# Optimization experiments

Hardware: AMD Instinct MI355X
Metric: run time of the kernel (lower is better)

The kernel has to match this reference:

```python
import jax, jax.numpy as jnp
import numpy as np

N, V, F, H, B, HID = 256, 32, 128, 8, 8, 64
R_MAX = 5.0
DH = F // H


def fc_edges(n):
    a = np.arange(n)
    s, r = np.meshgrid(a, a, indexing="ij")
    m = s != r
    return jnp.asarray(s[m]), jnp.asarray(r[m])

SENDERS, RECEIVERS = fc_edges(N)
E = N * (N - 1)


def sph_harmonics(u):
    # u: [..., 3] unit vectors -> [..., 15] = l=1(3)+l=2(5)+l=3(7), e3nn 'component' normalization
    x, y, z = u[..., 0], u[..., 1], u[..., 2]
    s3 = 3.0 ** 0.5; s5 = 5.0 ** 0.5; s7 = 7.0 ** 0.5
    s15 = 15.0 ** 0.5; s105 = 105.0 ** 0.5
    s35_8 = (35.0 / 8.0) ** 0.5; s21_8 = (21.0 / 8.0) ** 0.5
    l1 = [s3 * y, s3 * z, s3 * x]
    l2 = [s15 * x * y, s15 * y * z, 0.5 * s5 * (3 * z * z - 1),
          s15 * x * z, 0.5 * s15 * (x * x - y * y)]
    l3 = [s35_8 * y * (3 * x * x - y * y), s105 * x * y * z,
          s21_8 * y * (5 * z * z - 1), 0.5 * s7 * z * (5 * z * z - 3),
          s21_8 * x * (5 * z * z - 1), 0.5 * s105 * z * (x * x - y * y),
          s35_8 * x * (x * x - 3 * y * y)]
    return jnp.stack(l1 + l2 + l3, axis=-1)


def radial_embed(lengths):
    # Bessel basis (e3nn.bessel) times soft envelope (e3nn.soft_envelope)
    x = jnp.maximum(lengths, 1e-6)[..., None]
    k = jnp.arange(1, B + 1, dtype=lengths.dtype)
    bes = (2.0 / R_MAX) ** 0.5 * jnp.sin(k * jnp.pi * x / R_MAX) / x
    def sus(t):
        return jnp.where(t > 0, jnp.exp(-1.0 / jnp.where(t > 0, t, 1.0)), 0.0)
    env = 1.2 * sus(2.0 * (1.0 - lengths / R_MAX)) / sus(jnp.asarray(2.0))
    return bes * env[..., None]


def setup_inputs():
    key = jax.random.key(0)
    ks = jax.random.split(key, 16)
    def w(k, shape):
        return jax.random.normal(k, shape, jnp.float32) / (shape[0] ** 0.5)
    D_edge = 2 * F + V * B
    return {
        "positions": jax.random.normal(ks[0], (N, V, 3), jnp.float32),
        "features": jax.random.normal(ks[1], (N, F), jnp.float32),
        "We1": w(ks[2], (D_edge, HID)), "be1": jnp.zeros((HID,), jnp.float32),
        "We2": w(ks[3], (HID, HID)), "be2": jnp.zeros((HID,), jnp.float32),
        "W_q": w(ks[4], (F, F)), "W_k": w(ks[5], (HID, F)),
        "W_v": w(ks[6], (F, F)), "W_vec": w(ks[7], (HID, V)),
        "W_mix": w(ks[8], (V, V)),
        "M1": w(ks[9], (F, HID)), "bm1": jnp.zeros((HID,), jnp.float32),
        "M2": w(ks[10], (HID, HID)), "bm2": jnp.zeros((HID,), jnp.float32),
        "M3": w(ks[11], (HID, F)), "bm3": jnp.zeros((F,), jnp.float32),
    }


def reference(positions, features, We1, be1, We2, be2, W_q, W_k, W_v, W_vec,
              W_mix, M1, bm1, M2, bm2, M3, bm3):
    act = jax.nn.selu
    s, r = SENDERS, RECEIVERS
    vectors = positions[s] - positions[r]                        # [E, V, 3]
    lengths = jnp.sqrt(jnp.sum(vectors * vectors, -1) + 1e-18)   # [E, V] safe_norm
    unit = vectors / lengths[..., None]
    sph = sph_harmonics(unit)                                    # [E, V, 15]
    radial = radial_embed(lengths).reshape(E, V * B)             # [E, V*B]
    edge_weight_cutoff = jnp.ones((E,), positions.dtype)

    # edge MLP on invariants (radial embedding + src/dst scalar features)
    edge_in = jnp.concatenate([features[s], features[r], radial], -1)
    h = act(edge_in @ We1 + be1)
    h = act(h @ We2 + be2)                                       # [E, HID]

    # multi-head attention over incoming edges per node (segment softmax)
    q = (features @ W_q).reshape(N, H, DH)
    k = (h @ W_k).reshape(E, H, DH)
    logit = jnp.einsum("ehd,ehd->eh", k, q[r]) / (DH ** 0.5)
    lmax = jax.ops.segment_max(logit, r, num_segments=N)
    ex = edge_weight_cutoff[:, None] * jnp.exp(logit - lmax[r])
    denom = jax.ops.segment_sum(ex, r, num_segments=N)
    alpha = ex / (denom[r] + 1e-12)                              # [E, H]

    # invariant (0e) values
    v = (features[s] @ W_v).reshape(E, H, DH)
    inv_agg = jax.ops.segment_sum(alpha[..., None] * v, r, num_segments=N).reshape(N, F)

    # equivariant (1o) values: scalar-gated l=1 spherical harmonics (sqrt(3)*unit)
    coeff = h @ W_vec                                            # [E, V]
    alpha_v = jnp.repeat(alpha, V // H, axis=1)                  # [E, V]
    vec_msg = ((alpha_v * coeff) * (3.0 ** 0.5))[..., None] * unit  # [E, V, 3]
    vec_agg = jax.ops.segment_sum(vec_msg, r, num_segments=N)    # [N, V, 3]
    vec_out = jnp.einsum("nvc,vw->nwc", vec_agg, W_mix)

    # final invariant MLP + residuals
    hi = act(inv_agg @ M1 + bm1)
    hi = act(hi @ M2 + bm2)
    inv_out = hi @ M3 + bm3
    return (vec_out + positions, inv_out + features)
```

## Files before the change

kernel.cpp:

```cpp
#include <hip/hip_runtime.h>
#include <hip/hip_bf16.h>

#define NN 256
#define VC 32
#define FD 128

typedef unsigned int uint32;
typedef unsigned short u16;
typedef __attribute__((ext_vector_type(8))) short bf16x8;
typedef __attribute__((ext_vector_type(4))) float f32x4;

__device__ __forceinline__ float selu_f(float x) {
    const float lam = 1.0507009873554805f;
    const float la  = 1.7580993408473766f;
    return x > 0.f ? lam * x : la * (__expf(x) - 1.f);
}

__device__ __forceinline__ u16 f32_to_bf16_rne(float f) {
    uint32 u = __float_as_uint(f);
    uint32 r = (u + 0x7fffu + ((u >> 16) & 1u)) >> 16;
    return (u16)r;
}

__device__ __forceinline__ float bf16_to_f32(u16 h) {
    return __uint_as_float(((uint32)h) << 16);
}

struct Params {
    const float *pos, *feat, *We1, *be1, *We2, *be2, *Wq, *Wk, *Wv, *Wvec,
                *Wmix, *M1, *bm1, *M2, *bm2, *M3, *bm3;
    float *A, *Bf;
    u16 *kqb, *w1b, *we2b, *wvb, *fvtH, *fvtL, *ptH, *ptL;
    float *lgg2;
    u16 *cfg2;
    float *inv, *vec4;
    float *out0, *out1;
};

__global__ __launch_bounds__(256) void k1_pre(Params P)
{
    __shared__ float fl[FD];
    __shared__ float ql[FD];
    const int vb = blockIdx.x;
    const int t = threadIdx.x;
    if (vb < 256) {
        const int n = vb;
        {
            const int gid = n*256 + t;
            if (gid < 16384) {
                const int c = gid >> 8, k = gid & 255;
                P.w1b[gid] = f32_to_bf16_rne(P.We1[(256 + k)*64 + c]);
            } else if (gid < 20480) {
                const int o = gid - 16384;
                const int c = o >> 6, k = o & 63;
                P.we2b[o] = f32_to_bf16_rne(P.We2[k*64 + c]);
            } else if (gid < 22528) {
                const int o = gid - 20480;
                const int v = o >> 6, k = o & 63;
                P.wvb[o] = f32_to_bf16_rne(P.Wvec[k*32 + v]);
            }
        }
        if (t < FD) fl[t] = P.feat[n*FD + t];
        __syncthreads();
        if (t < 64) {
            float a = 0.f;
            for (int i = 0; i < FD; ++i) a = fmaf(fl[i], P.We1[i*64 + t], a);
            P.A[n*64 + t] = a;
        } else if (t < 128) {
            const int j = t - 64;
            float a = P.be1[j];
            for (int i = 0; i < FD; ++i) a = fmaf(fl[i], P.We1[(FD+i)*64 + j], a);
            P.Bf[n*64 + j] = a;
        } else {
            const int j = t - 128;
            float a = 0.f;
            for (int i = 0; i < FD; ++i) a = fmaf(fl[i], P.Wq[i*FD + j], a);
            ql[j] = a * 0.25f;
        }
        if (t < 8)  P.lgg2[n*2048 + t*256 + n] = -1e30f;
        if (t < 32) P.cfg2[(size_t)n*8192 + t*256 + n] = 0;
        __syncthreads();
        for (int o = t; o < 512; o += 256) {
            const int h = o >> 6, j = o & 63;
            float a = 0.f;
            #pragma unroll
            for (int d = 0; d < 16; ++d)
                a = fmaf(P.Wk[j*FD + h*16 + d], ql[h*16 + d], a);
            P.kqb[n*512 + o] = f32_to_bf16_rne(a);
        }
    } else {
        const int n = vb - 256;
        if (t < FD) fl[t] = P.feat[n*FD + t];
        __syncthreads();
        if (t < FD) {
            float a = 0.f;
            for (int i = 0; i < FD; ++i) a = fmaf(fl[i], P.Wv[i*FD + t], a);
            const u16 hi = f32_to_bf16_rne(a);
            const u16 lo = f32_to_bf16_rne(a - bf16_to_f32(hi));
            P.fvtH[t*256 + n] = hi;
            P.fvtL[t*256 + n] = lo;
            const int v = t >> 2, c = t & 3;
            const float val = (c < 3) ? P.pos[(n*VC + v)*3 + c] : 1.0f;
            const u16 phi = f32_to_bf16_rne(val);
            const u16 plo = f32_to_bf16_rne(val - bf16_to_f32(phi));
            P.ptH[(v*4+c)*256 + n] = phi;
            P.ptL[(v*4+c)*256 + n] = plo;
        }
    }
}

__global__ __launch_bounds__(256) void k2_edge(Params P)
{
    __shared__ u16 rad[8192];
    __shared__ u16 h1b[2048];
    __shared__ u16 h2b[2048];
    __shared__ float invl[1056];

    const int t = threadIdx.x;
    const int wave = t >> 6, l = t & 63;
    const int li = l & 15, q = l >> 4;
    const int mh = wave >> 1, eh = wave & 1;
    const int r = blockIdx.x >> 1, tpart = blockIdx.x & 1;
    const int e = eh*16 + li;
    const int swz16 = (e & 7) << 3;

    bf16x8 w1A[2][8];
    #pragma unroll
    for (int mt = 0; mt < 2; ++mt) {
        const int c = mh*32 + mt*16 + li;
        #pragma unroll
        for (int kb = 0; kb < 8; ++kb)
            w1A[mt][kb] = *(const bf16x8*)(P.w1b + c*256 + kb*32 + q*8);
    }
    bf16x8 we2A[2][2];
    #pragma unroll
    for (int mt = 0; mt < 2; ++mt) {
        const int c2 = mh*32 + mt*16 + li;
        #pragma unroll
        for (int kb = 0; kb < 2; ++kb)
            we2A[mt][kb] = *(const bf16x8*)(P.we2b + c2*64 + kb*32 + q*8);
    }
    bf16x8 wvA[2];
    {
        const int v = mh*16 + li;
        #pragma unroll
        for (int kb = 0; kb < 2; ++kb)
            wvA[kb] = *(const bf16x8*)(P.wvb + v*64 + kb*32 + q*8);
    }
    bf16x8 kqA[2];
    if (li < 8) {
        #pragma unroll
        for (int kb = 0; kb < 2; ++kb)
            kqA[kb] = *(const bf16x8*)(P.kqb + r*512 + li*64 + kb*32 + q*8);
    } else {
        #pragma unroll
        for (int kb = 0; kb < 2; ++kb)
            #pragma unroll
            for (int j = 0; j < 8; ++j) kqA[kb][j] = 0;
    }
    float bfreg[2][4], be2reg[2][4];
    #pragma unroll
    for (int mt = 0; mt < 2; ++mt)
        #pragma unroll
        for (int rg = 0; rg < 4; ++rg) {
            const int c = mh*32 + mt*16 + q*4 + rg;
            bfreg[mt][rg] = P.Bf[r*64 + c];
            be2reg[mt][rg] = P.be2[c];
        }

    for (int it = 0; it < 4; ++it) {
        const int s0 = (tpart*4 + it) * 32;
        const int sp = s0 + e;
        int s = sp + (sp >= r ? 1 : 0); if (s > 255) s = 255;
        __syncthreads();

        float As[2][4];
        #pragma unroll
        for (int mt = 0; mt < 2; ++mt)
            #pragma unroll
            for (int rg = 0; rg < 4; ++rg)
                As[mt][rg] = P.A[s*64 + mh*32 + mt*16 + q*4 + rg];

        {
            const int ep = t & 31, vg = t >> 5;
            const int spp = s0 + ep;
            int sv = spp + (spp >= r ? 1 : 0); if (sv > 255) sv = 255;
            #pragma unroll
            for (int kk = 0; kk < 4; ++kk) {
                const int v = vg*4 + kk;
                const float* ps = P.pos + (sv*VC + v)*3;
                const float* pr = P.pos + (r*VC + v)*3;
                const float dx = ps[0]-pr[0], dy = ps[1]-pr[1], dz = ps[2]-pr[2];
                const float d2 = fmaf(dx,dx,fmaf(dy,dy,dz*dz)) + 1e-18f;
                const float len = sqrtf(d2);
                invl[ep*33 + v] = rsqrtf(d2);
                const float x = fmaxf(len, 1e-6f);
                const float tt2 = 2.f - 0.4f*len;
                const float env = tt2 > 0.f ? 1.9784655248401538f * __expf(-1.f/tt2) : 0.f;
                const float coefc = 0.6324555320336759f * env / x;
                float s_cur, c1;
                __sincosf(0.6283185307179586f * x, &s_cur, &c1);
                const float c2x = 2.f * c1;
                float s_prev = 0.f;
                union { uint4 u4; u16 us[8]; } pk;
                #pragma unroll
                for (int bb = 0; bb < 8; ++bb) {
                    pk.us[bb] = f32_to_bf16_rne(coefc * s_cur);
                    const float s_next = fmaf(c2x, s_cur, -s_prev);
                    s_prev = s_cur; s_cur = s_next;
                }
                *(uint4*)((char*)rad + ((ep*512 + v*16) ^ ((ep & 15) << 4))) = pk.u4;
            }
        }
        __syncthreads();

        f32x4 d1[2] = {{0.f,0.f,0.f,0.f},{0.f,0.f,0.f,0.f}};
        #pragma unroll
        for (int kb = 0; kb < 8; ++kb) {
            const bf16x8 rf = *(const bf16x8*)((const char*)rad +
                                ((e*512 + (kb*4+q)*16) ^ ((e & 15) << 4)));
            d1[0] = __builtin_amdgcn_mfma_f32_16x16x32_bf16(w1A[0][kb], rf, d1[0], 0, 0, 0);
            d1[1] = __builtin_amdgcn_mfma_f32_16x16x32_bf16(w1A[1][kb], rf, d1[1], 0, 0, 0);
        }
        #pragma unroll
        for (int mt = 0; mt < 2; ++mt) {
            const int c0 = mh*32 + mt*16 + q*4;
            const u16 p0 = f32_to_bf16_rne(selu_f(d1[mt][0] + As[mt][0] + bfreg[mt][0]));
            const u16 p1 = f32_to_bf16_rne(selu_f(d1[mt][1] + As[mt][1] + bfreg[mt][1]));
            const u16 p2 = f32_to_bf16_rne(selu_f(d1[mt][2] + As[mt][2] + bfreg[mt][2]));
            const u16 p3 = f32_to_bf16_rne(selu_f(d1[mt][3] + As[mt][3] + bfreg[mt][3]));
            *(uint32*)&h1b[e*64 + ((c0)     ^ swz16)] = (uint32)p0 | ((uint32)p1 << 16);
            *(uint32*)&h1b[e*64 + ((c0 + 2) ^ swz16)] = (uint32)p2 | ((uint32)p3 << 16);
        }
        __syncthreads();

        f32x4 d2[2] = {{0.f,0.f,0.f,0.f},{0.f,0.f,0.f,0.f}};
        #pragma unroll
        for (int kb = 0; kb < 2; ++kb) {
            const bf16x8 hb = *(const bf16x8*)&h1b[e*64 + ((kb*32 + q*8) ^ swz16)];
            d2[0] = __builtin_amdgcn_mfma_f32_16x16x32_bf16(we2A[0][kb], hb, d2[0], 0, 0, 0);
            d2[1] = __builtin_amdgcn_mfma_f32_16x16x32_bf16(we2A[1][kb], hb, d2[1], 0, 0, 0);
        }
        #pragma unroll
        for (int mt = 0; mt < 2; ++mt) {
            const int c0 = mh*32 + mt*16 + q*4;
            const u16 p0 = f32_to_bf16_rne(selu_f(d2[mt][0] + be2reg[mt][0]));
            const u16 p1 = f32_to_bf16_rne(selu_f(d2[mt][1] + be2reg[mt][1]));
            const u16 p2 = f32_to_bf16_rne(selu_f(d2[mt][2] + be2reg[mt][2]));
            const u16 p3 = f32_to_bf16_rne(selu_f(d2[mt][3] + be2reg[mt][3]));
            *(uint32*)&h2b[e*64 + ((c0)     ^ swz16)] = (uint32)p0 | ((uint32)p1 << 16);
            *(uint32*)&h2b[e*64 + ((c0 + 2) ^ swz16)] = (uint32)p2 | ((uint32)p3 << 16);
        }
        __syncthreads();

        f32x4 d3 = {0.f,0.f,0.f,0.f};
        f32x4 dl = {0.f,0.f,0.f,0.f};
        #pragma unroll
        for (int kb = 0; kb < 2; ++kb) {
            const bf16x8 hb = *(const bf16x8*)&h2b[e*64 + ((kb*32 + q*8) ^ swz16)];
            d3 = __builtin_amdgcn_mfma_f32_16x16x32_bf16(wvA[kb], hb, d3, 0, 0, 0);
            if (mh == 0)
                dl = __builtin_amdgcn_mfma_f32_16x16x32_bf16(kqA[kb], hb, dl, 0, 0, 0);
        }
        if (sp < 255) {
            #pragma unroll
            for (int rg = 0; rg < 4; ++rg) {
                const int v = mh*16 + q*4 + rg;
                P.cfg2[(size_t)r*8192 + v*256 + s] =
                    f32_to_bf16_rne(d3[rg] * 1.7320508075688772f * invl[e*33 + v]);
            }
            if (mh == 0 && q < 2) {
                #pragma unroll
                for (int rg = 0; rg < 4; ++rg)
                    P.lgg2[(size_t)r*2048 + (q*4+rg)*256 + s] = dl[rg];
            }
        }
    }
}

__global__ __launch_bounds__(64) void k3b_agg(Params P)
{
    const int l = threadIdx.x, li = l & 15, q = l >> 4;
    const int task = blockIdx.x;
    if (task < 128) {
        const int h = task >> 4, r0 = (task & 15) * 16;
        bf16x8 fH[8], fL[8];
        #pragma unroll
        for (int kb = 0; kb < 8; ++kb) {
            fH[kb] = *(const bf16x8*)(P.fvtH + (h*16+li)*256 + kb*32 + q*8);
            fL[kb] = *(const bf16x8*)(P.fvtL + (h*16+li)*256 + kb*32 + q*8);
        }
        const float* lgr = P.lgg2 + (size_t)(r0+li)*2048 + h*256;
        float mx = -3.0e38f;
        #pragma unroll
        for (int kb = 0; kb < 8; ++kb) {
            const float4 g0 = *(const float4*)(lgr + kb*32 + q*8);
            const float4 g1 = *(const float4*)(lgr + kb*32 + q*8 + 4);
            mx = fmaxf(mx, fmaxf(fmaxf(g0.x,g0.y), fmaxf(g0.z,g0.w)));
            mx = fmaxf(mx, fmaxf(fmaxf(g1.x,g1.y), fmaxf(g1.z,g1.w)));
        }
        mx = fmaxf(mx, __shfl_xor(mx, 16));
        mx = fmaxf(mx, __shfl_xor(mx, 32));
        float ssum = 0.f;
        f32x4 Ch = {0.f,0.f,0.f,0.f};
        f32x4 Cl = {0.f,0.f,0.f,0.f};
        #pragma unroll
        for (int kb = 0; kb < 8; ++kb) {
            const float4 g0 = *(const float4*)(lgr + kb*32 + q*8);
            const float4 g1 = *(const float4*)(lgr + kb*32 + q*8 + 4);
            float ev[8];
            ev[0]=__expf(g0.x-mx); ev[1]=__expf(g0.y-mx); ev[2]=__expf(g0.z-mx); ev[3]=__expf(g0.w-mx);
            ev[4]=__expf(g1.x-mx); ev[5]=__expf(g1.y-mx); ev[6]=__expf(g1.z-mx); ev[7]=__expf(g1.w-mx);
            bf16x8 a;
            #pragma unroll
            for (int j = 0; j < 8; ++j) { ssum += ev[j]; a[j] = (short)f32_to_bf16_rne(ev[j]); }
            Ch = __builtin_amdgcn_mfma_f32_16x16x32_bf16(a, fH[kb], Ch, 0, 0, 0);
            Cl = __builtin_amdgcn_mfma_f32_16x16x32_bf16(a, fL[kb], Cl, 0, 0, 0);
        }
        ssum += __shfl_xor(ssum, 16);
        ssum += __shfl_xor(ssum, 32);
        #pragma unroll
        for (int rg = 0; rg < 4; ++rg) {
            const float d = __shfl(ssum, q*4 + rg);
            P.inv[(r0 + q*4 + rg)*128 + h*16 + li] = (Ch[rg] + Cl[rg]) / (d + 1e-12f);
        }
    } else {
        const int b2 = task - 128, v = b2 >> 4, r0 = (b2 & 15) * 16;
        const int h = v >> 2;
        bf16x8 pH[8], pL[8];
        #pragma unroll
        for (int kb = 0; kb < 8; ++kb) {
            if (li < 4) {
                pH[kb] = *(const bf16x8*)(P.ptH + (v*4+li)*256 + kb*32 + q*8);
                pL[kb] = *(const bf16x8*)(P.ptL + (v*4+li)*256 + kb*32 + q*8);
            } else {
                #pragma unroll
                for (int j = 0; j < 8; ++j) { pH[kb][j] = 0; pL[kb][j] = 0; }
            }
        }
        const float* lgr = P.lgg2 + (size_t)(r0+li)*2048 + h*256;
        const u16*  cfr = P.cfg2 + (size_t)(r0+li)*8192 + v*256;
        float mx = -3.0e38f;
        #pragma unroll
        for (int kb = 0; kb < 8; ++kb) {
            const float4 g0 = *(const float4*)(lgr + kb*32 + q*8);
            const float4 g1 = *(const float4*)(lgr + kb*32 + q*8 + 4);
            mx = fmaxf(mx, fmaxf(fmaxf(g0.x,g0.y), fmaxf(g0.z,g0.w)));
            mx = fmaxf(mx, fmaxf(fmaxf(g1.x,g1.y), fmaxf(g1.z,g1.w)));
        }
        mx = fmaxf(mx, __shfl_xor(mx, 16));
        mx = fmaxf(mx, __shfl_xor(mx, 32));
        float ssum = 0.f;
        f32x4 Ch = {0.f,0.f,0.f,0.f};
        f32x4 Cl = {0.f,0.f,0.f,0.f};
        #pragma unroll
        for (int kb = 0; kb < 8; ++kb) {
            const float4 g0 = *(const float4*)(lgr + kb*32 + q*8);
            const float4 g1 = *(const float4*)(lgr + kb*32 + q*8 + 4);
            const bf16x8 cf8 = *(const bf16x8*)(cfr + kb*32 + q*8);
            float ev[8];
            ev[0]=__expf(g0.x-mx); ev[1]=__expf(g0.y-mx); ev[2]=__expf(g0.z-mx); ev[3]=__expf(g0.w-mx);
            ev[4]=__expf(g1.x-mx); ev[5]=__expf(g1.y-mx); ev[6]=__expf(g1.z-mx); ev[7]=__expf(g1.w-mx);
            bf16x8 a;
            #pragma unroll
            for (int j = 0; j < 8; ++j) {
                ssum += ev[j];
                a[j] = (short)f32_to_bf16_rne(ev[j] * bf16_to_f32((u16)cf8[j]));
            }
            Ch = __builtin_amdgcn_mfma_f32_16x16x32_bf16(a, pH[kb], Ch, 0, 0, 0);
            Cl = __builtin_amdgcn_mfma_f32_16x16x32_bf16(a, pL[kb], Cl, 0, 0, 0);
        }
        ssum += __shfl_xor(ssum, 16);
        ssum += __shfl_xor(ssum, 32);
        #pragma unroll
        for (int rg = 0; rg < 4; ++rg) {
            const float d = __shfl(ssum, q*4 + rg);
            if (li < 4)
                P.vec4[(r0 + q*4 + rg)*128 + v*4 + li] = (Ch[rg] + Cl[rg]) / (d + 1e-12f);
        }
    }
}

__global__ __launch_bounds__(256) void k3c_out(Params P)
{
    __shared__ float part[4][64];
    __shared__ float inva[128];
    __shared__ float vec4s[128];
    __shared__ float pos96[96];
    __shared__ float vecl[96];
    __shared__ float hi1[64];
    __shared__ float hi2[64];
    const int r = blockIdx.x;
    const int t = threadIdx.x;
    if (t < 128) inva[t] = P.inv[r*128 + t];
    else         vec4s[t-128] = P.vec4[r*128 + (t-128)];
    if (t < 96)  pos96[t] = P.pos[r*96 + t];
    __syncthreads();
    if (t < 96) {
        const int v = t / 3, c = t - v*3;
        vecl[t] = vec4s[v*4 + c] - vec4s[v*4 + 3] * pos96[t];
    }
    {
        const int f = t & 63, g = t >> 6;
        const int k0 = g*32;
        float acc = 0.f;
        #pragma unroll 8
        for (int k = k0; k < k0 + 32; ++k)
            acc = fmaf(inva[k], P.M1[k*64 + f], acc);
        part[g][f] = acc;
    }
    __syncthreads();
    if (t < 64) {
        const float a1 = P.bm1[t] + part[0][t] + part[1][t] + part[2][t] + part[3][t];
        hi1[t] = selu_f(a1);
    }
    __syncthreads();
    if (t < 64) {
        float a2 = P.bm2[t];
        #pragma unroll 8
        for (int k = 0; k < 64; ++k) a2 = fmaf(hi1[k], P.M2[k*64 + t], a2);
        hi2[t] = selu_f(a2);
    }
    __syncthreads();
    if (t < 128) {
        float a = P.bm3[t];
        #pragma unroll 8
        for (int k = 0; k < 64; ++k) a = fmaf(hi2[k], P.M3[k*128 + t], a);
        P.out1[r*128 + t] = a + P.feat[r*128 + t];
    } else if (t < 224) {
        const int o = t - 128;
        const int w = o / 3, c = o - w*3;
        float a = 0.f;
        #pragma unroll
        for (int v = 0; v < 32; ++v)
            a = fmaf(vecl[v*3 + c], P.Wmix[v*32 + w], a);
        P.out0[r*96 + o] = a + pos96[o];
    }
}

extern "C" void kernel_launch(void* const* d_in, const int* in_sizes, int n_in,
                              void* d_out, int out_size, void* d_ws, size_t ws_size,
                              hipStream_t stream)
{
    char* ws = (char*)d_ws;
    if (ws_size < (size_t)6991872) return;

    Params p;
    p.pos  = (const float*)d_in[0];
    p.feat = (const float*)d_in[1];
    p.We1  = (const float*)d_in[2];
    p.be1  = (const float*)d_in[3];
    p.We2  = (const float*)d_in[4];
    p.be2  = (const float*)d_in[5];
    p.Wq   = (const float*)d_in[6];
    p.Wk   = (const float*)d_in[7];
    p.Wv   = (const float*)d_in[8];
    p.Wvec = (const float*)d_in[9];
    p.Wmix = (const float*)d_in[10];
    p.M1   = (const float*)d_in[11];
    p.bm1  = (const float*)d_in[12];
    p.M2   = (const float*)d_in[13];
    p.bm2  = (const float*)d_in[14];
    p.M3   = (const float*)d_in[15];
    p.bm3  = (const float*)d_in[16];

    p.A    = (float*)(ws + 0);
    p.Bf   = (float*)(ws + 65536);
    p.kqb  = (u16*)(ws + 131072);
    p.w1b  = (u16*)(ws + 393216);
    p.we2b = (u16*)(ws + 425984);
    p.wvb  = (u16*)(ws + 434176);
    p.fvtH = (u16*)(ws + 438272);
    p.fvtL = (u16*)(ws + 503808);
    p.ptH  = (u16*)(ws + 569344);
    p.ptL  = (u16*)(ws + 634880);
    p.lgg2 = (float*)(ws + 700416);
    p.cfg2 = (u16*)(ws + 2797568);
    p.inv  = (float*)(ws + 0);
    p.vec4 = (float*)(ws + 131072);

    p.out0 = (float*)d_out;
    p.out1 = p.out0 + NN*VC*3;

    hipLaunchKernelGGL(k1_pre,  dim3(512), dim3(256), 0, stream, p);
    hipLaunchKernelGGL(k2_edge, dim3(512), dim3(256), 0, stream, p);
    hipLaunchKernelGGL(k3b_agg, dim3(640), dim3(64),  0, stream, p);
    hipLaunchKernelGGL(k3c_out, dim3(256), dim3(256), 0, stream, p);
}
```

Baseline: 44.56 us.

## Compute online softmax max/sum stats in edge kernel, drop max pass in aggregation

The edge kernel now keeps a running max and rescaled exp-sum (online softmax) for each receiver and head as it produces logits. It reduces these across lanes and waves and writes per-block partial stats to a new workspace buffer. The aggregation kernel merges the two partials instead of making a separate max pass over the logits and summing exps itself, so it does one fewer read of the logit array and fewer reductions. In exchange the edge kernel does extra exp work, shuffles and a block sync, and the denominator is now taken from fp32 exps rather than from the same exps fed to the MFMA.

```diff
diff --git a/kernel.cpp b/kernel.cpp
--- a/kernel.cpp
+++ b/kernel.cpp
@@ -33,6 +33,7 @@
     u16 *kqb, *w1b, *we2b, *wvb, *fvtH, *fvtL, *ptH, *ptL;
     float *lgg2;
     u16 *cfg2;
+    float *stats;
     float *inv, *vec4;
     float *out0, *out1;
 };
@@ -115,6 +116,8 @@
     __shared__ u16 h1b[2048];
     __shared__ u16 h2b[2048];
     __shared__ float invl[1056];
+    __shared__ float pm[2][8];
+    __shared__ float psv[2][8];
 
     const int t = threadIdx.x;
     const int wave = t >> 6, l = t & 63;
@@ -167,6 +170,10 @@
             bfreg[mt][rg] = P.Bf[r*64 + c];
             be2reg[mt][rg] = P.be2[c];
         }
+
+    float m_run[4], s_run[4];
+    #pragma unroll
+    for (int rg = 0; rg < 4; ++rg) { m_run[rg] = -3.0e38f; s_run[rg] = 0.f; }
 
     for (int it = 0; it < 4; ++it) {
         const int s0 = (tpart*4 + it) * 32;
@@ -271,10 +278,44 @@
             }
             if (mh == 0 && q < 2) {
                 #pragma unroll
-                for (int rg = 0; rg < 4; ++rg)
-                    P.lgg2[(size_t)r*2048 + (q*4+rg)*256 + s] = dl[rg];
+                for (int rg = 0; rg < 4; ++rg) {
+                    const float lgv = dl[rg];
+                    P.lgg2[(size_t)r*2048 + (q*4+rg)*256 + s] = lgv;
+                    const float mo = m_run[rg];
+                    if (lgv > mo) {
+                        s_run[rg] = fmaf(s_run[rg], __expf(mo - lgv), 1.f);
+                        m_run[rg] = lgv;
+                    } else {
+                        s_run[rg] += __expf(lgv - mo);
+                    }
+                }
             }
         }
+    }
+
+    if (mh == 0 && q < 2) {
+        #pragma unroll
+        for (int rg = 0; rg < 4; ++rg) {
+            float m = m_run[rg], sv = s_run[rg];
+            #pragma unroll
+            for (int mask = 1; mask <= 8; mask <<= 1) {
+                const float mo = __shfl_xor(m, mask);
+                const float so = __shfl_xor(sv, mask);
+                const float mn = fmaxf(m, mo);
+                sv = sv*__expf(m - mn) + so*__expf(mo - mn);
+                m = mn;
+            }
+            if (li == 0) { pm[eh][q*4+rg] = m; psv[eh][q*4+rg] = sv; }
+        }
+    }
+    __syncthreads();
+    if (t < 8) {
+        const float m0 = pm[0][t], m1 = pm[1][t];
+        const float s0v = psv[0][t], s1v = psv[1][t];
+        const float m = fmaxf(m0, m1);
+        const float sv = s0v*__expf(m0 - m) + s1v*__expf(m1 - m);
+        P.stats[((r*2 + tpart)*8 + t)*2 + 0] = m;
+        P.stats[((r*2 + tpart)*8 + t)*2 + 1] = sv;
     }
 }
 
@@ -282,51 +323,49 @@
 {
     const int l = threadIdx.x, li = l & 15, q = l >> 4;
     const int task = blockIdx.x;
-    if (task < 128) {
-        const int h = task >> 4, r0 = (task & 15) * 16;
+    int r0, hh, v = 0;
+    const bool isInv = (task < 128);
+    if (isInv) { hh = task >> 4; r0 = (task & 15) * 16; }
+    else { const int b2 = task - 128; v = b2 >> 4; r0 = (b2 & 15) * 16; hh = v >> 2; }
+
+    const float2 st0 = *(const float2*)&P.stats[(((r0+li)*2 + 0)*8 + hh)*2];
+    const float2 st1 = *(const float2*)&P.stats[(((r0+li)*2 + 1)*8 + hh)*2];
+    const float mx = fmaxf(st0.x, st1.x);
+    const float den = st0.y*__expf(st0.x - mx) + st1.y*__expf(st1.x - mx);
+    const float invden = 1.f / (den + 1e-12f);
+
+    if (isInv) {
         bf16x8 fH[8], fL[8];
         #pragma unroll
         for (int kb = 0; kb < 8; ++kb) {
-            fH[kb] = *(const bf16x8*)(P.fvtH + (h*16+li)*256 + kb*32 + q*8);
-            fL[kb] = *(const bf16x8*)(P.fvtL + (h*16+li)*256 + kb*32 + q*8);
-        }
-        const float* lgr = P.lgg2 + (size_t)(r0+li)*2048 + h*256;
-        float mx = -3.0e38f;
+            fH[kb] = *(const bf16x8*)(P.fvtH + (hh*16+li)*256 + kb*32 + q*8);
+            fL[kb] = *(const bf16x8*)(P.fvtL + (hh*16+li)*256 + kb*32 + q*8);
+        }
+        const float* lgr = P.lgg2 + (size_t)(r0+li)*2048 + hh*256;
+        f32x4 Ch = {0.f,0.f,0.f,0.f};
+        f32x4 Cl = {0.f,0.f,0.f,0.f};
         #pragma unroll
         for (int kb = 0; kb < 8; ++kb) {
             const float4 g0 = *(const float4*)(lgr + kb*32 + q*8);
             const float4 g1 = *(const float4*)(lgr + kb*32 + q*8 + 4);
-            mx = fmaxf(mx, fmaxf(fmaxf(g0.x,g0.y), fmaxf(g0.z,g0.w)));
-            mx = fmaxf(mx, fmaxf(fmaxf(g1.x,g1.y), fmaxf(g1.z,g1.w)));
-        }
-        mx = fmaxf(mx, __shfl_xor(mx, 16));
-        mx = fmaxf(mx, __shfl_xor(mx, 32));
-        float ssum = 0.f;
-        f32x4 Ch = {0.f,0.f,0.f,0.f};
-        f32x4 Cl = {0.f,0.f,0.f,0.f};
-        #pragma unroll
-        for (int kb = 0; kb < 8; ++kb) {
-            const float4 g0 = *(const float4*)(lgr + kb*32 + q*8);
-            const float4 g1 = *(const float4*)(lgr + kb*32 + q*8 + 4);
-            float ev[8];
-            ev[0]=__expf(g0.x-mx); ev[1]=__expf(g0.y-mx); ev[2]=__expf(g0.z-mx); ev[3]=__expf(g0.w-mx);
-            ev[4]=__expf(g1.x-mx); ev[5]=__expf(g1.y-mx); ev[6]=__expf(g1.z-mx); ev[7]=__expf(g1.w-mx);
             bf16x8 a;
-            #pragma unroll
-            for (int j = 0; j < 8; ++j) { ssum += ev[j]; a[j] = (short)f32_to_bf16_rne(ev[j]); }
+            a[0] = (short)f32_to_bf16_rne(__expf(g0.x-mx));
+            a[1] = (short)f32_to_bf16_rne(__expf(g0.y-mx));
+            a[2] = (short)f32_to_bf16_rne(__expf(g0.z-mx));
+            a[3] = (short)f32_to_bf16_rne(__expf(g0.w-mx));
+            a[4] = (short)f32_to_bf16_rne(__expf(g1.x-mx));
+            a[5] = (short)f32_to_bf16_rne(__expf(g1.y-mx));
+            a[6] = (short)f32_to_bf16_rne(__expf(g1.z-mx));
+            a[7] = (short)f32_to_bf16_rne(__expf(g1.w-mx));
             Ch = __builtin_amdgcn_mfma_f32_16x16x32_bf16(a, fH[kb], Ch, 0, 0, 0);
             Cl = __builtin_amdgcn_mfma_f32_16x16x32_bf16(a, fL[kb], Cl, 0, 0, 0);
         }
-        ssum += __shfl_xor(ssum, 16);
-        ssum += __shfl_xor(ssum, 32);
         #pragma unroll
         for (int rg = 0; rg < 4; ++rg) {
-            const float d = __shfl(ssum, q*4 + rg);
-            P.inv[(r0 + q*4 + rg)*128 + h*16 + li] = (Ch[rg] + Cl[rg]) / (d + 1e-12f);
+            const float d = __shfl(invden, q*4 + rg);
+            P.inv[(r0 + q*4 + rg)*128 + hh*16 + li] = (Ch[rg] + Cl[rg]) * d;
         }
     } else {
-        const int b2 = task - 128, v = b2 >> 4, r0 = (b2 & 15) * 16;
-        const int h = v >> 2;
         bf16x8 pH[8], pL[8];
         #pragma unroll
         for (int kb = 0; kb < 8; ++kb) {
@@ -338,19 +377,8 @@
                 for (int j = 0; j < 8; ++j) { pH[kb][j] = 0; pL[kb][j] = 0; }
             }
         }
-        const float* lgr = P.lgg2 + (size_t)(r0+li)*2048 + h*256;
+        const float* lgr = P.lgg2 + (size_t)(r0+li)*2048 + hh*256;
         const u16*  cfr = P.cfg2 + (size_t)(r0+li)*8192 + v*256;
-        float mx = -3.0e38f;
-        #pragma unroll
-        for (int kb = 0; kb < 8; ++kb) {
-            const float4 g0 = *(const float4*)(lgr + kb*32 + q*8);
-            const float4 g1 = *(const float4*)(lgr + kb*32 + q*8 + 4);
-            mx = fmaxf(mx, fmaxf(fmaxf(g0.x,g0.y), fmaxf(g0.z,g0.w)));
-            mx = fmaxf(mx, fmaxf(fmaxf(g1.x,g1.y), fmaxf(g1.z,g1.w)));
-        }
-        mx = fmaxf(mx, __shfl_xor(mx, 16));
-        mx = fmaxf(mx, __shfl_xor(mx, 32));
-        float ssum = 0.f;
         f32x4 Ch = {0.f,0.f,0.f,0.f};
         f32x4 Cl = {0.f,0.f,0.f,0.f};
         #pragma unroll
@@ -358,25 +386,23 @@
             const float4 g0 = *(const float4*)(lgr + kb*32 + q*8);
             const float4 g1 = *(const float4*)(lgr + kb*32 + q*8 + 4);
             const bf16x8 cf8 = *(const bf16x8*)(cfr + kb*32 + q*8);
-            float ev[8];
-            ev[0]=__expf(g0.x-mx); ev[1]=__expf(g0.y-mx); ev[2]=__expf(g0.z-mx); ev[3]=__expf(g0.w-mx);
-            ev[4]=__expf(g1.x-mx); ev[5]=__expf(g1.y-mx); ev[6]=__expf(g1.z-mx); ev[7]=__expf(g1.w-mx);
             bf16x8 a;
-            #pragma unroll
-            for (int j = 0; j < 8; ++j) {
-                ssum += ev[j];
-                a[j] = (short)f32_to_bf16_rne(ev[j] * bf16_to_f32((u16)cf8[j]));
-            }
+            a[0] = (short)f32_to_bf16_rne(__expf(g0.x-mx) * bf16_to_f32((u16)cf8[0]));
+            a[1] = (short)f32_to_bf16_rne(__expf(g0.y-mx) * bf16_to_f32((u16)cf8[1]));
+            a[2] = (short)f32_to_bf16_rne(__expf(g0.z-mx) * bf16_to_f32((u16)cf8[2]));
+            a[3] = (short)f32_to_bf16_rne(__expf(g0.w-mx) * bf16_to_f32((u16)cf8[3]));
+            a[4] = (short)f32_to_bf16_rne(__expf(g1.x-mx) * bf16_to_f32((u16)cf8[4]));
+            a[5] = (short)f32_to_bf16_rne(__expf(g1.y-mx) * bf16_to_f32((u16)cf8[5]));
+            a[6] = (short)f32_to_bf16_rne(__expf(g1.z-mx) * bf16_to_f32((u16)cf8[6]));
+            a[7] = (short)f32_to_bf16_rne(__expf(g1.w-mx) * bf16_to_f32((u16)cf8[7]));
             Ch = __builtin_amdgcn_mfma_f32_16x16x32_bf16(a, pH[kb], Ch, 0, 0, 0);
             Cl = __builtin_amdgcn_mfma_f32_16x16x32_bf16(a, pL[kb], Cl, 0, 0, 0);
         }
-        ssum += __shfl_xor(ssum, 16);
-        ssum += __shfl_xor(ssum, 32);
         #pragma unroll
         for (int rg = 0; rg < 4; ++rg) {
-            const float d = __shfl(ssum, q*4 + rg);
+            const float d = __shfl(invden, q*4 + rg);
             if (li < 4)
-                P.vec4[(r0 + q*4 + rg)*128 + v*4 + li] = (Ch[rg] + Cl[rg]) / (d + 1e-12f);
+                P.vec4[(r0 + q*4 + rg)*128 + v*4 + li] = (Ch[rg] + Cl[rg]) * d;
         }
     }
 }
@@ -443,7 +469,7 @@
                               hipStream_t stream)
 {
     char* ws = (char*)d_ws;
-    if (ws_size < (size_t)6991872) return;
+    if (ws_size < (size_t)7024640) return;
 
     Params p;
     p.pos  = (const float*)d_in[0];
@@ -476,6 +502,7 @@
     p.ptL  = (u16*)(ws + 634880);
     p.lgg2 = (float*)(ws + 700416);
     p.cfg2 = (u16*)(ws + 2797568);
+    p.stats = (float*)(ws + 6991872);
     p.inv  = (float*)(ws + 0);
     p.vec4 = (float*)(ws + 131072);
 
```

Result: slower. 45.58 us (+2.3%).
